# Performance work log

Hardware: AMD Instinct MI355X
Metric: run time of the kernel (lower is better)

The kernel has to match this reference:

```python
import jax, jax.numpy as jnp
import numpy as np

N, G, H = 500_000, 25_000, 256


def setup_inputs() -> dict:
    key = jax.random.key(0)
    ks = jax.random.split(key, 8)
    node = jax.random.normal(ks[0], (N, H), dtype=jnp.float32)
    super_node = jax.random.normal(ks[1], (G, H), dtype=jnp.float32)
    segment_ids = jnp.sort(jax.random.randint(ks[2], (N,), 0, G, dtype=jnp.int32))
    s = 0.05
    return {
        "node": node,
        "super_node": super_node,
        "segment_ids": segment_ids,
        "w_align": jax.random.normal(ks[3], (2 * H, 1), jnp.float32) * s,
        "b_align": jnp.zeros((1,), jnp.float32),
        "w_attend": jax.random.normal(ks[4], (H, H), jnp.float32) * s,
        "b_attend": jnp.zeros((H,), jnp.float32),
        "w_ih": jax.random.normal(ks[5], (H, 3 * H), jnp.float32) * s,
        "w_hh": jax.random.normal(ks[6], (H, 3 * H), jnp.float32) * s,
        "b_ih": jnp.zeros((3 * H,), jnp.float32),
        "b_hh": jnp.zeros((3 * H,), jnp.float32),
    }


def reference(node, super_node, segment_ids, w_align, b_align, w_attend,
              b_attend, w_ih, w_hh, b_ih, b_hh):
    g = super_node.shape[0]
    h = node.shape[1]
    # super_node = F.leaky_relu(super_node)
    s = jax.nn.leaky_relu(super_node)  # slope 0.01 (torch default)
    # cal_alignment(cat([node, broadcast_nodes(super)])) == node@Wn + (s@Ws)[seg]
    wn, ws = w_align[:h], w_align[h:]
    score = jax.nn.leaky_relu(node @ wn + (s @ ws)[segment_ids] + b_align)  # [N,1]
    # softmax_nodes: segment-wise stable softmax
    m = jax.ops.segment_max(score, segment_ids, num_segments=g)
    w = jnp.exp(score - m[segment_ids])
    denom = jax.ops.segment_sum(w, segment_ids, num_segments=g)
    attn = w / denom[segment_ids]  # [N,1]
    # attend (dropout=0, eval)
    hidden = node @ w_attend + b_attend  # [N,H]
    # sum_nodes weighted by attention, then ELU
    ctx = jax.nn.elu(jax.ops.segment_sum(attn * hidden, segment_ids, num_segments=g))  # [G,H]
    # GRUCell(ctx, s) per torch semantics
    gi = ctx @ w_ih + b_ih
    gh = s @ w_hh + b_hh
    ir, iz, inn = jnp.split(gi, 3, axis=-1)
    hr, hz, hn = jnp.split(gh, 3, axis=-1)
    r = jax.nn.sigmoid(ir + hr)
    z = jax.nn.sigmoid(iz + hz)
    n = jnp.tanh(inn + r * hn)
    new_h = (1.0 - z) * n + z * s
    return jax.nn.relu(new_h), attn
```

## Files before the change

### kernel.cpp

```cpp
#include <hip/hip_runtime.h>
#include <math.h>

#define N_NODES 500000
#define G_SEG   25000
#define H_DIM   256
#define SPB     4

typedef __attribute__((ext_vector_type(4))) float f32x4;
typedef __attribute__((ext_vector_type(8))) short bf16x8;

__device__ __forceinline__ float leaky(float x){ return x > 0.f ? x : 0.01f * x; }

__device__ __forceinline__ ushort f2bf(float f){
  unsigned u = __float_as_uint(f);
  u += 0x7FFFu + ((u >> 16) & 1u);
  return (ushort)(u >> 16);
}

__global__ __launch_bounds__(256) void k_starts(
    const int* __restrict__ seg, int* __restrict__ starts)
{
  int i = blockIdx.x * 256 + threadIdx.x;
  if (i >= N_NODES) return;
  int s = seg[i];
  int prev = (i == 0) ? -1 : seg[i - 1];
  for (int g = prev + 1; g <= s; g++) starts[g] = i;
  if (i == N_NODES - 1)
    for (int g = s + 1; g <= G_SEG; g++) starts[g] = N_NODES;
}

__global__ __launch_bounds__(256) void kPack(
    const float* __restrict__ w_att, const float* __restrict__ w_ih,
    const float* __restrict__ w_hh, ushort* __restrict__ Bp,
    ushort* __restrict__ Bp6)
{
  int b = blockIdx.x, c = threadIdx.x;
  if (b < 256) {
    int kk = b;
    Bp[(((kk >> 3) << 8) + c) * 8 + (kk & 7)] = f2bf(w_att[kk * H_DIM + c]);
  } else {
    int kk = b - 256;
    #pragma unroll
    for (int gate = 0; gate < 4; gate++) {
      float v;
      if (gate == 0)      v = (kk < 256) ? w_ih[kk * 768 + c]        : w_hh[(kk - 256) * 768 + c];
      else if (gate == 1) v = (kk < 256) ? w_ih[kk * 768 + 256 + c]  : w_hh[(kk - 256) * 768 + 256 + c];
      else if (gate == 2) v = (kk < 256) ? w_ih[kk * 768 + 512 + c]  : 0.f;
      else                v = (kk < 256) ? 0.f                       : w_hh[(kk - 256) * 768 + 512 + c];
      int n = (gate << 8) + c;
      Bp6[(((kk >> 3) << 10) + n) * 8 + (kk & 7)] = f2bf(v);
    }
  }
}

__global__ __launch_bounds__(256) void k1_prep_super(
    const float* __restrict__ sn, const float* __restrict__ w_align,
    float* __restrict__ s_buf, float* __restrict__ sws)
{
  int g = blockIdx.x, t = threadIdx.x;
  float v = sn[g * H_DIM + t];
  float sv = leaky(v);
  s_buf[g * H_DIM + t] = sv;
  float p = sv * w_align[H_DIM + t];
  #pragma unroll
  for (int d = 1; d < 64; d <<= 1) p += __shfl_xor(p, d);
  __shared__ float red[4];
  int wid = t >> 6, lane = t & 63;
  if (lane == 0) red[wid] = p;
  __syncthreads();
  if (t == 0) sws[g] = red[0] + red[1] + red[2] + red[3];
}

__global__ __launch_bounds__(256) void kF_score_softmax_agg(
    const float* __restrict__ node, const int* __restrict__ starts,
    const float* __restrict__ w_align, const float* __restrict__ b_align,
    const float* __restrict__ sws,
    float* __restrict__ attn_out, float* __restrict__ agg,
    float* __restrict__ bscale)
{
  __shared__ int st_s[SPB + 1];
  const int tid = threadIdx.x;
  const int g0 = blockIdx.x * SPB;
  if (tid <= SPB) st_s[tid] = starts[g0 + tid];
  __syncthreads();

  const int wv = tid >> 6, lane = tid & 63;
  const float4 wvec = ((const float4*)w_align)[lane];
  const float b0 = b_align[0];

  const int g  = g0 + wv;
  const int st = st_s[wv], en = st_s[wv + 1];
  const float swsg = sws[g];

  float m = -3.4e38f, sum = 0.f;
  f32x4 pacc = {0.f, 0.f, 0.f, 0.f};

  int r = st;
  for (; r + 3 < en; r += 4) {
    f32x4 a0 = ((const f32x4*)node)[(size_t)(r    ) * 64 + lane];
    f32x4 a1 = ((const f32x4*)node)[(size_t)(r + 1) * 64 + lane];
    f32x4 a2 = ((const f32x4*)node)[(size_t)(r + 2) * 64 + lane];
    f32x4 a3 = ((const f32x4*)node)[(size_t)(r + 3) * 64 + lane];
    float d0 = a0[0]*wvec.x + a0[1]*wvec.y + a0[2]*wvec.z + a0[3]*wvec.w;
    float d1 = a1[0]*wvec.x + a1[1]*wvec.y + a1[2]*wvec.z + a1[3]*wvec.w;
    float d2 = a2[0]*wvec.x + a2[1]*wvec.y + a2[2]*wvec.z + a2[3]*wvec.w;
    float d3 = a3[0]*wvec.x + a3[1]*wvec.y + a3[2]*wvec.z + a3[3]*wvec.w;
    #pragma unroll
    for (int s2 = 1; s2 < 64; s2 <<= 1) {
      d0 += __shfl_xor(d0, s2);
      d1 += __shfl_xor(d1, s2);
      d2 += __shfl_xor(d2, s2);
      d3 += __shfl_xor(d3, s2);
    }
    float sc0 = leaky(d0 + swsg + b0);
    float sc1 = leaky(d1 + swsg + b0);
    float sc2 = leaky(d2 + swsg + b0);
    float sc3 = leaky(d3 + swsg + b0);
    if (lane < 4) {
      float scs = (lane == 0) ? sc0 : (lane == 1) ? sc1 : (lane == 2) ? sc2 : sc3;
      attn_out[r + lane] = scs;
    }
    float bm = fmaxf(fmaxf(sc0, sc1), fmaxf(sc2, sc3));
    if (bm > m) {
      float scale = __expf(m - bm);
      sum *= scale; pacc *= scale; m = bm;
    }
    float p0 = __expf(sc0 - m), p1 = __expf(sc1 - m);
    float p2 = __expf(sc2 - m), p3 = __expf(sc3 - m);
    sum += (p0 + p1) + (p2 + p3);
    pacc += p0 * a0 + p1 * a1;
    pacc += p2 * a2 + p3 * a3;
  }
  for (; r < en; r++) {
    f32x4 a = ((const f32x4*)node)[(size_t)r * 64 + lane];
    float d = a[0]*wvec.x + a[1]*wvec.y + a[2]*wvec.z + a[3]*wvec.w;
    #pragma unroll
    for (int s2 = 1; s2 < 64; s2 <<= 1) d += __shfl_xor(d, s2);
    float sc = leaky(d + swsg + b0);
    if (lane == 0) attn_out[r] = sc;
    if (sc <= m) {
      float p = __expf(sc - m);
      sum += p;
      pacc += p * a;
    } else {
      float scale = __expf(m - sc);
      sum = sum * scale + 1.f;
      pacc = pacc * scale + a;
      m = sc;
    }
  }

  float invD = (sum > 0.f) ? 1.f / sum : 0.f;
  ((f32x4*)(agg + (size_t)g * H_DIM))[lane] = pacc * invD;
  if (lane == 0) bscale[g] = (sum > 0.f) ? 1.f : 0.f;
  for (int rr = st + lane; rr < en; rr += 64)
    attn_out[rr] = __expf(attn_out[rr] - m) * invD;
}

__global__ __launch_bounds__(256, 2) void k5b_ctx(
    const float* __restrict__ agg, const ushort* __restrict__ Bp,
    const float* __restrict__ b_att, const float* __restrict__ bscale,
    float* __restrict__ ctx)
{
  __shared__ __align__(16) ushort A_lds[128 * 256];

  const int tid  = threadIdx.x;
  const int row0 = blockIdx.x * 128;

  #pragma unroll
  for (int i = 0; i < 16; i++) {
    int v = tid + i * 256;
    int r = v >> 5;
    int s = v & 31;
    int grow = row0 + r;
    f32x4 x0 = {0.f, 0.f, 0.f, 0.f}, x1 = {0.f, 0.f, 0.f, 0.f};
    if (grow < G_SEG) {
      const f32x4* p = (const f32x4*)(agg + (size_t)grow * H_DIM) + s * 2;
      x0 = p[0]; x1 = p[1];
    }
    bf16x8 t;
    t[0] = (short)f2bf(x0[0]); t[1] = (short)f2bf(x0[1]);
    t[2] = (short)f2bf(x0[2]); t[3] = (short)f2bf(x0[3]);
    t[4] = (short)f2bf(x1[0]); t[5] = (short)f2bf(x1[1]);
    t[6] = (short)f2bf(x1[2]); t[7] = (short)f2bf(x1[3]);
    *(bf16x8*)&A_lds[r * 256 + ((s ^ (r & 7)) * 8)] = t;
  }
  __syncthreads();

  const int wv  = tid >> 6;
  const int l   = tid & 63;
  const int l15 = l & 15, lq = l >> 4, l7 = l & 7;
  const int colbase = wv * 64 + l15;

  f32x4 acc[8][4];
  #pragma unroll
  for (int mf = 0; mf < 8; mf++)
    #pragma unroll
    for (int nf = 0; nf < 4; nf++)
      acc[mf][nf] = (f32x4){0.f, 0.f, 0.f, 0.f};

  for (int ks = 0; ks < 8; ks++) {
    int c = ks * 4 + lq;
    bf16x8 b[4];
    #pragma unroll
    for (int nf = 0; nf < 4; nf++)
      b[nf] = *(const bf16x8*)&Bp[(((c << 8) + colbase + nf * 16)) * 8];
    bf16x8 a[8];
    #pragma unroll
    for (int mf = 0; mf < 8; mf++)
      a[mf] = *(const bf16x8*)&A_lds[(mf * 16 + l15) * 256 + ((c ^ l7) * 8)];
    #pragma unroll
    for (int mf = 0; mf < 8; mf++)
      #pragma unroll
      for (int nf = 0; nf < 4; nf++)
        acc[mf][nf] = __builtin_amdgcn_mfma_f32_16x16x32_bf16(
            a[mf], b[nf], acc[mf][nf], 0, 0, 0);
  }

  float bias[4];
  #pragma unroll
  for (int nf = 0; nf < 4; nf++) bias[nf] = b_att[colbase + nf * 16];

  #pragma unroll
  for (int mf = 0; mf < 8; mf++) {
    #pragma unroll
    for (int r = 0; r < 4; r++) {
      int grow = row0 + mf * 16 + lq * 4 + r;
      if (grow < G_SEG) {
        float bsc = bscale[grow];
        #pragma unroll
        for (int nf = 0; nf < 4; nf++)
          ctx[(size_t)grow * H_DIM + colbase + nf * 16] =
              acc[mf][nf][r] + bias[nf] * bsc;
      }
    }
  }
}

__global__ __launch_bounds__(256, 2) void k6_mfma(
    const float* __restrict__ ctxbuf, const float* __restrict__ s_buf,
    const ushort* __restrict__ Bp6,
    const float* __restrict__ b_ih, const float* __restrict__ b_hh,
    float* __restrict__ out0)
{
  __shared__ __align__(16) ushort A_lds[32 * 512];

  const int tid  = threadIdx.x;
  const int row0 = blockIdx.x * 32;

  #pragma unroll
  for (int i = 0; i < 8; i++) {
    int v = tid + i * 256;
    int r = v >> 6;
    int s = v & 63;
    int g = row0 + r;
    f32x4 x0 = {0.f, 0.f, 0.f, 0.f}, x1 = {0.f, 0.f, 0.f, 0.f};
    if (g < G_SEG) {
      const f32x4* p = (s < 32)
          ? (const f32x4*)(ctxbuf + (size_t)g * H_DIM) + s * 2
          : (const f32x4*)(s_buf + (size_t)g * H_DIM) + (s - 32) * 2;
      x0 = p[0]; x1 = p[1];
      if (s < 32) {
        #pragma unroll
        for (int e = 0; e < 4; e++) {
          x0[e] = x0[e] > 0.f ? x0[e] : (__expf(x0[e]) - 1.f);
          x1[e] = x1[e] > 0.f ? x1[e] : (__expf(x1[e]) - 1.f);
        }
      }
    }
    bf16x8 t;
    t[0] = (short)f2bf(x0[0]); t[1] = (short)f2bf(x0[1]);
    t[2] = (short)f2bf(x0[2]); t[3] = (short)f2bf(x0[3]);
    t[4] = (short)f2bf(x1[0]); t[5] = (short)f2bf(x1[1]);
    t[6] = (short)f2bf(x1[2]); t[7] = (short)f2bf(x1[3]);
    *(bf16x8*)&A_lds[r * 512 + ((s ^ (r & 7)) * 8)] = t;
  }
  __syncthreads();

  const int wv  = tid >> 6;
  const int l   = tid & 63;
  const int l15 = l & 15, lq = l >> 4, l7 = l & 7;

  f32x4 acc[4][2][4];
  #pragma unroll
  for (int gt = 0; gt < 4; gt++)
    #pragma unroll
    for (int mf = 0; mf < 2; mf++)
      #pragma unroll
      for (int nf = 0; nf < 4; nf++)
        acc[gt][mf][nf] = (f32x4){0.f, 0.f, 0.f, 0.f};

  for (int ks = 0; ks < 16; ks++) {
    int c = ks * 4 + lq;
    bf16x8 a[2];
    #pragma unroll
    for (int mf = 0; mf < 2; mf++)
      a[mf] = *(const bf16x8*)&A_lds[(mf * 16 + l15) * 512 + ((c ^ l7) * 8)];
    #pragma unroll
    for (int gt = 0; gt < 4; gt++) {
      if (gt == 2 && ks >= 8) continue;
      if (gt == 3 && ks < 8) continue;
      #pragma unroll
      for (int nf = 0; nf < 4; nf++) {
        int n = (gt << 8) + (wv << 6) + nf * 16 + l15;
        bf16x8 b = *(const bf16x8*)&Bp6[(((c << 10) + n)) * 8];
        acc[gt][0][nf] = __builtin_amdgcn_mfma_f32_16x16x32_bf16(
            a[0], b, acc[gt][0][nf], 0, 0, 0);
        acc[gt][1][nf] = __builtin_amdgcn_mfma_f32_16x16x32_bf16(
            a[1], b, acc[gt][1][nf], 0, 0, 0);
      }
    }
  }

  #pragma unroll
  for (int nf = 0; nf < 4; nf++) {
    int cc = (wv << 6) + nf * 16 + l15;
    float bir = b_ih[cc] + b_hh[cc];
    float biz = b_ih[256 + cc] + b_hh[256 + cc];
    float bin_ = b_ih[512 + cc];
    float bhn  = b_hh[512 + cc];
    #pragma unroll
    for (int mf = 0; mf < 2; mf++) {
      #pragma unroll
      for (int rr = 0; rr < 4; rr++) {
        int grow = row0 + mf * 16 + lq * 4 + rr;
        if (grow < G_SEG) {
          float v0 = acc[0][mf][nf][rr];
          float v1 = acc[1][mf][nf][rr];
          float v2 = acc[2][mf][nf][rr];
          float v3 = acc[3][mf][nf][rr];
          float r_ = 1.f / (1.f + __expf(-(v0 + bir)));
          float z_ = 1.f / (1.f + __expf(-(v1 + biz)));
          float n_ = tanhf(v2 + bin_ + r_ * (v3 + bhn));
          float sv = s_buf[(size_t)grow * H_DIM + cc];
          float nh = (1.f - z_) * n_ + z_ * sv;
          out0[(size_t)grow * H_DIM + cc] = nh > 0.f ? nh : 0.f;
        }
      }
    }
  }
}

extern "C" void kernel_launch(void* const* d_in, const int* in_sizes, int n_in,
                              void* d_out, int out_size, void* d_ws, size_t ws_size,
                              hipStream_t stream)
{
  (void)in_sizes; (void)n_in; (void)out_size; (void)ws_size;
  const float* node       = (const float*)d_in[0];
  const float* super_node = (const float*)d_in[1];
  const int*   seg        = (const int*)d_in[2];
  const float* w_align    = (const float*)d_in[3];
  const float* b_align    = (const float*)d_in[4];
  const float* w_att      = (const float*)d_in[5];
  const float* b_att      = (const float*)d_in[6];
  const float* w_ih       = (const float*)d_in[7];
  const float* w_hh       = (const float*)d_in[8];
  const float* b_ih       = (const float*)d_in[9];
  const float* b_hh       = (const float*)d_in[10];

  float* out0     = (float*)d_out;
  float* attn_out = (float*)d_out + (size_t)G_SEG * H_DIM;

  float* ws     = (float*)d_ws;
  float* s_buf  = ws;
  float* sws    = ws + 6400000;
  float* agg    = ws + 6425000;
  ushort* Bp    = (ushort*)(ws + 12825000);
  ushort* Bp6   = (ushort*)(ws + 12860000);
  float* bscale = ws + 13125000;
  int*   starts = (int*)(ws + 13150000);
  float* ctx    = ws + 13200000;

  k_starts<<<(N_NODES + 255) / 256, 256, 0, stream>>>(seg, starts);
  kPack<<<768, 256, 0, stream>>>(w_att, w_ih, w_hh, Bp, Bp6);
  k1_prep_super<<<G_SEG, 256, 0, stream>>>(super_node, w_align, s_buf, sws);
  kF_score_softmax_agg<<<G_SEG / SPB, 256, 0, stream>>>(
      node, starts, w_align, b_align, sws, attn_out, agg, bscale);
  k5b_ctx<<<(G_SEG + 127) / 128, 256, 0, stream>>>(agg, Bp, b_att, bscale, ctx);
  k6_mfma<<<(G_SEG + 31) / 32, 256, 0, stream>>>(ctx, s_buf, Bp6, b_ih, b_hh, out0);
}
```

Baseline: 270.4 us.

## Fuse prep kernels, transpose-reduce score shuffles, enlarge GRU MFMA tile

Merges the segment-start, weight-packing and super-node prep kernels into one launch, which removes two kernel launches and their serialization. In the score loop, the four full butterfly reductions are replaced by a transpose-style reduction in which each of lanes 0-3 ends up holding one row's score, with exps computed once and broadcast by shuffle. The GRU MFMA kernel now processes 64 rows per 512-thread block so each block reuses the packed weights across twice as many rows. The trade-offs are a larger LDS footprint per block and more shuffle dependencies in the hot loop.

```diff
diff --git a/kernel.cpp b/kernel.cpp
--- a/kernel.cpp
+++ b/kernel.cpp
@@ -17,58 +17,57 @@
   return (ushort)(u >> 16);
 }
 
-__global__ __launch_bounds__(256) void k_starts(
-    const int* __restrict__ seg, int* __restrict__ starts)
-{
-  int i = blockIdx.x * 256 + threadIdx.x;
-  if (i >= N_NODES) return;
-  int s = seg[i];
-  int prev = (i == 0) ? -1 : seg[i - 1];
-  for (int g = prev + 1; g <= s; g++) starts[g] = i;
-  if (i == N_NODES - 1)
-    for (int g = s + 1; g <= G_SEG; g++) starts[g] = N_NODES;
-}
-
-__global__ __launch_bounds__(256) void kPack(
-    const float* __restrict__ w_att, const float* __restrict__ w_ih,
-    const float* __restrict__ w_hh, ushort* __restrict__ Bp,
+__global__ __launch_bounds__(256) void kPrep(
+    const float* __restrict__ sn, const float* __restrict__ w_align,
+    const int* __restrict__ seg, const float* __restrict__ w_att,
+    const float* __restrict__ w_ih, const float* __restrict__ w_hh,
+    float* __restrict__ s_buf, float* __restrict__ sws,
+    int* __restrict__ starts, ushort* __restrict__ Bp,
     ushort* __restrict__ Bp6)
 {
-  int b = blockIdx.x, c = threadIdx.x;
-  if (b < 256) {
-    int kk = b;
-    Bp[(((kk >> 3) << 8) + c) * 8 + (kk & 7)] = f2bf(w_att[kk * H_DIM + c]);
-  } else {
-    int kk = b - 256;
+  int b = blockIdx.x, t = threadIdx.x;
+
+  {
+    float v = sn[b * H_DIM + t];
+    float sv = leaky(v);
+    s_buf[b * H_DIM + t] = sv;
+    float p = sv * w_align[H_DIM + t];
+    #pragma unroll
+    for (int d = 1; d < 64; d <<= 1) p += __shfl_xor(p, d);
+    __shared__ float red[4];
+    int wid = t >> 6, lane = t & 63;
+    if (lane == 0) red[wid] = p;
+    __syncthreads();
+    if (t == 0) sws[b] = red[0] + red[1] + red[2] + red[3];
+  }
+
+  if (b < 1954) {
+    int i = b * 256 + t;
+    if (i < N_NODES) {
+      int s = seg[i];
+      int prev = (i == 0) ? -1 : seg[i - 1];
+      for (int g = prev + 1; g <= s; g++) starts[g] = i;
+      if (i == N_NODES - 1)
+        for (int g = s + 1; g <= G_SEG; g++) starts[g] = N_NODES;
+    }
+  }
+  else if (b >= 2000 && b < 2256) {
+    int kk = b - 2000;
+    Bp[(((kk >> 3) << 8) + t) * 8 + (kk & 7)] = f2bf(w_att[kk * H_DIM + t]);
+  }
+  else if (b >= 2256 && b < 2768) {
+    int kk = b - 2256;
     #pragma unroll
     for (int gate = 0; gate < 4; gate++) {
       float v;
-      if (gate == 0)      v = (kk < 256) ? w_ih[kk * 768 + c]        : w_hh[(kk - 256) * 768 + c];
-      else if (gate == 1) v = (kk < 256) ? w_ih[kk * 768 + 256 + c]  : w_hh[(kk - 256) * 768 + 256 + c];
-      else if (gate == 2) v = (kk < 256) ? w_ih[kk * 768 + 512 + c]  : 0.f;
-      else                v = (kk < 256) ? 0.f                       : w_hh[(kk - 256) * 768 + 512 + c];
-      int n = (gate << 8) + c;
+      if (gate == 0)      v = (kk < 256) ? w_ih[kk * 768 + t]        : w_hh[(kk - 256) * 768 + t];
+      else if (gate == 1) v = (kk < 256) ? w_ih[kk * 768 + 256 + t]  : w_hh[(kk - 256) * 768 + 256 + t];
+      else if (gate == 2) v = (kk < 256) ? w_ih[kk * 768 + 512 + t]  : 0.f;
+      else                v = (kk < 256) ? 0.f                       : w_hh[(kk - 256) * 768 + 512 + t];
+      int n = (gate << 8) + t;
       Bp6[(((kk >> 3) << 10) + n) * 8 + (kk & 7)] = f2bf(v);
     }
   }
-}
-
-__global__ __launch_bounds__(256) void k1_prep_super(
-    const float* __restrict__ sn, const float* __restrict__ w_align,
-    float* __restrict__ s_buf, float* __restrict__ sws)
-{
-  int g = blockIdx.x, t = threadIdx.x;
-  float v = sn[g * H_DIM + t];
-  float sv = leaky(v);
-  s_buf[g * H_DIM + t] = sv;
-  float p = sv * w_align[H_DIM + t];
-  #pragma unroll
-  for (int d = 1; d < 64; d <<= 1) p += __shfl_xor(p, d);
-  __shared__ float red[4];
-  int wid = t >> 6, lane = t & 63;
-  if (lane == 0) red[wid] = p;
-  __syncthreads();
-  if (t == 0) sws[g] = red[0] + red[1] + red[2] + red[3];
 }
 
 __global__ __launch_bounds__(256) void kF_score_softmax_agg(
@@ -105,28 +104,35 @@
     float d1 = a1[0]*wvec.x + a1[1]*wvec.y + a1[2]*wvec.z + a1[3]*wvec.w;
     float d2 = a2[0]*wvec.x + a2[1]*wvec.y + a2[2]*wvec.z + a2[3]*wvec.w;
     float d3 = a3[0]*wvec.x + a3[1]*wvec.y + a3[2]*wvec.z + a3[3]*wvec.w;
-    #pragma unroll
-    for (int s2 = 1; s2 < 64; s2 <<= 1) {
-      d0 += __shfl_xor(d0, s2);
-      d1 += __shfl_xor(d1, s2);
-      d2 += __shfl_xor(d2, s2);
-      d3 += __shfl_xor(d3, s2);
-    }
-    float sc0 = leaky(d0 + swsg + b0);
-    float sc1 = leaky(d1 + swsg + b0);
-    float sc2 = leaky(d2 + swsg + b0);
-    float sc3 = leaky(d3 + swsg + b0);
-    if (lane < 4) {
-      float scs = (lane == 0) ? sc0 : (lane == 1) ? sc1 : (lane == 2) ? sc2 : sc3;
-      attn_out[r + lane] = scs;
-    }
-    float bm = fmaxf(fmaxf(sc0, sc1), fmaxf(sc2, sc3));
+
+    float k01 = (lane & 1) ? d1 : d0;
+    float s01 = (lane & 1) ? d0 : d1;
+    k01 += __shfl_xor(s01, 1);
+    float k23 = (lane & 1) ? d3 : d2;
+    float s23 = (lane & 1) ? d2 : d3;
+    k23 += __shfl_xor(s23, 1);
+    float x  = (lane & 2) ? k23 : k01;
+    float xs = (lane & 2) ? k01 : k23;
+    x += __shfl_xor(xs, 2);
+    x += __shfl_xor(x, 4);
+    x += __shfl_xor(x, 8);
+    x += __shfl_xor(x, 16);
+    x += __shfl_xor(x, 32);
+
+    float sc = leaky(x + swsg + b0);
+    if (lane < 4) attn_out[r + lane] = sc;
+
+    float bm = fmaxf(sc, __shfl_xor(sc, 1));
+    bm = fmaxf(bm, __shfl_xor(bm, 2));
     if (bm > m) {
       float scale = __expf(m - bm);
       sum *= scale; pacc *= scale; m = bm;
     }
-    float p0 = __expf(sc0 - m), p1 = __expf(sc1 - m);
-    float p2 = __expf(sc2 - m), p3 = __expf(sc3 - m);
+    float p = __expf(sc - m);
+    float p0 = __shfl(p, 0);
+    float p1 = __shfl(p, 1);
+    float p2 = __shfl(p, 2);
+    float p3 = __shfl(p, 3);
     sum += (p0 + p1) + (p2 + p3);
     pacc += p0 * a0 + p1 * a1;
     pacc += p2 * a2 + p3 * a3;
@@ -237,20 +243,20 @@
   }
 }
 
-__global__ __launch_bounds__(256, 2) void k6_mfma(
+__global__ __launch_bounds__(512, 2) void k6_mfma(
     const float* __restrict__ ctxbuf, const float* __restrict__ s_buf,
     const ushort* __restrict__ Bp6,
     const float* __restrict__ b_ih, const float* __restrict__ b_hh,
     float* __restrict__ out0)
 {
-  __shared__ __align__(16) ushort A_lds[32 * 512];
+  __shared__ __align__(16) ushort A_lds[64 * 512];
 
   const int tid  = threadIdx.x;
-  const int row0 = blockIdx.x * 32;
+  const int row0 = blockIdx.x * 64;
 
   #pragma unroll
   for (int i = 0; i < 8; i++) {
-    int v = tid + i * 256;
+    int v = tid + i * 512;
     int r = v >> 6;
     int s = v & 63;
     int g = row0 + r;
@@ -278,6 +284,8 @@
   __syncthreads();
 
   const int wv  = tid >> 6;
+  const int rh  = (wv >> 2) * 32;
+  const int cw  = (wv & 3) << 6;
   const int l   = tid & 63;
   const int l15 = l & 15, lq = l >> 4, l7 = l & 7;
 
@@ -295,14 +303,14 @@
     bf16x8 a[2];
     #pragma unroll
     for (int mf = 0; mf < 2; mf++)
-      a[mf] = *(const bf16x8*)&A_lds[(mf * 16 + l15) * 512 + ((c ^ l7) * 8)];
+      a[mf] = *(const bf16x8*)&A_lds[(rh + mf * 16 + l15) * 512 + ((c ^ l7) * 8)];
     #pragma unroll
     for (int gt = 0; gt < 4; gt++) {
       if (gt == 2 && ks >= 8) continue;
       if (gt == 3 && ks < 8) continue;
       #pragma unroll
       for (int nf = 0; nf < 4; nf++) {
-        int n = (gt << 8) + (wv << 6) + nf * 16 + l15;
+        int n = (gt << 8) + cw + nf * 16 + l15;
         bf16x8 b = *(const bf16x8*)&Bp6[(((c << 10) + n)) * 8];
         acc[gt][0][nf] = __builtin_amdgcn_mfma_f32_16x16x32_bf16(
             a[0], b, acc[gt][0][nf], 0, 0, 0);
@@ -314,7 +322,7 @@
 
   #pragma unroll
   for (int nf = 0; nf < 4; nf++) {
-    int cc = (wv << 6) + nf * 16 + l15;
+    int cc = cw + nf * 16 + l15;
     float bir = b_ih[cc] + b_hh[cc];
     float biz = b_ih[256 + cc] + b_hh[256 + cc];
     float bin_ = b_ih[512 + cc];
@@ -323,7 +331,7 @@
     for (int mf = 0; mf < 2; mf++) {
       #pragma unroll
       for (int rr = 0; rr < 4; rr++) {
-        int grow = row0 + mf * 16 + lq * 4 + rr;
+        int grow = row0 + rh + mf * 16 + lq * 4 + rr;
         if (grow < G_SEG) {
           float v0 = acc[0][mf][nf][rr];
           float v1 = acc[1][mf][nf][rr];
@@ -371,11 +379,10 @@
   int*   starts = (int*)(ws + 13150000);
   float* ctx    = ws + 13200000;
 
-  k_starts<<<(N_NODES + 255) / 256, 256, 0, stream>>>(seg, starts);
-  kPack<<<768, 256, 0, stream>>>(w_att, w_ih, w_hh, Bp, Bp6);
-  k1_prep_super<<<G_SEG, 256, 0, stream>>>(super_node, w_align, s_buf, sws);
+  kPrep<<<G_SEG, 256, 0, stream>>>(super_node, w_align, seg, w_att, w_ih, w_hh,
+                                   s_buf, sws, starts, Bp, Bp6);
   kF_score_softmax_agg<<<G_SEG / SPB, 256, 0, stream>>>(
       node, starts, w_align, b_align, sws, attn_out, agg, bscale);
   k5b_ctx<<<(G_SEG + 127) / 128, 256, 0, stream>>>(agg, Bp, b_att, bscale, ctx);
-  k6_mfma<<<(G_SEG + 31) / 32, 256, 0, stream>>>(ctx, s_buf, Bp6, b_ih, b_hh, out0);
-}
+  k6_mfma<<<(G_SEG + 63) / 64, 512, 0, stream>>>(ctx, s_buf, Bp6, b_ih, b_hh, out0);
+}
```

Measured after the change: 263.4 us. -2.6%, faster.
